# Kernel optimization log

Measured on AMD Instinct MI355X. Metric: run time of the kernel, lower is better.

The kernel has to match this reference:

```python
import jax, jax.numpy as jnp
import numpy as np

B, IN_CH, N, DIM, PH, HID, K = 4, 128, 2048, 256, 64, 1024, 16
EPS = 1e-5


def conv1(x, w, b):
    # 1x1 Conv1d: x (B,C,N), w (O,C) -> (B,O,N)
    return jnp.einsum('oc,bcn->bon', w, x) + b[None, :, None]


def conv2(x, w, b):
    # 1x1 Conv2d: x (B,C,N,K), w (O,C) -> (B,O,N,K)
    return jnp.einsum('oc,bcnk->bonk', w, x) + b[None, :, None, None]


def bn2(x, g, beta, mean, var):
    # eval-mode BatchNorm2d over channel dim of (B,C,N,K)
    scale = g * jax.lax.rsqrt(var + EPS)
    return x * scale[None, :, None, None] + (beta - mean * scale)[None, :, None, None]


def query_knn(pos, k):
    # pos: (B,3,N). Returns (B,N,K) indices of k nearest neighbors (incl. self).
    p = jnp.transpose(pos, (0, 2, 1))                     # (B,N,3)
    sq = jnp.sum(p * p, axis=-1)                          # (B,N)
    dist = sq[:, :, None] + sq[:, None, :] - 2.0 * jnp.einsum('bnc,bmc->bnm', p, p)
    _, idx = jax.lax.top_k(-dist, k)                      # smallest distances first
    return idx


def group(feat, idx):
    # feat: (B,C,N), idx: (B,N,K) -> (B,C,N,K) where out[b,c,i,k]=feat[b,c,idx[b,i,k]]
    b, c, n = feat.shape
    k = idx.shape[-1]
    ib = jnp.broadcast_to(idx.reshape(b, 1, n * k), (b, c, n * k))
    return jnp.take_along_axis(feat, ib, axis=2).reshape(b, c, n, k)


def setup_inputs() -> dict:
    key = jax.random.key(0)
    ks = jax.random.split(key, 12)
    s = 0.02
    return {
        'x': jax.random.normal(ks[0], (B, IN_CH, N), jnp.float32),
        'pos': jax.random.normal(ks[1], (B, 3, N), jnp.float32),
        'ls_w': jax.random.normal(ks[2], (DIM, IN_CH), jnp.float32) * s,
        'ls_b': jnp.zeros((DIM,), jnp.float32),
        'kw': jax.random.normal(ks[3], (DIM, DIM), jnp.float32) * s,
        'kb': jnp.zeros((DIM,), jnp.float32),
        'qw': jax.random.normal(ks[4], (DIM, DIM), jnp.float32) * s,
        'qb': jnp.zeros((DIM,), jnp.float32),
        'vw': jax.random.normal(ks[5], (DIM, DIM), jnp.float32) * s,
        'vb': jnp.zeros((DIM,), jnp.float32),
        'pw1': jax.random.normal(ks[6], (PH, 3), jnp.float32) * s,
        'pb1': jnp.zeros((PH,), jnp.float32),
        'pg': jnp.ones((PH,), jnp.float32),
        'pbeta': jnp.zeros((PH,), jnp.float32),
        'pmean': jnp.zeros((PH,), jnp.float32),
        'pvar': jnp.ones((PH,), jnp.float32),
        'pw2': jax.random.normal(ks[7], (DIM, PH), jnp.float32) * s,
        'pb2': jnp.zeros((DIM,), jnp.float32),
        'aw1': jax.random.normal(ks[8], (HID, DIM), jnp.float32) * s,
        'ab1': jnp.zeros((HID,), jnp.float32),
        'ag': jnp.ones((HID,), jnp.float32),
        'abeta': jnp.zeros((HID,), jnp.float32),
        'amean': jnp.zeros((HID,), jnp.float32),
        'avar': jnp.ones((HID,), jnp.float32),
        'aw2': jax.random.normal(ks[9], (DIM, HID), jnp.float32) * s,
        'ab2': jnp.zeros((DIM,), jnp.float32),
        'lw': jax.random.normal(ks[10], (IN_CH, DIM), jnp.float32) * s,
        'lb': jnp.zeros((IN_CH,), jnp.float32),
    }


def reference(x, pos, ls_w, ls_b, kw, kb, qw, qb, vw, vb,
              pw1, pb1, pg, pbeta, pmean, pvar, pw2, pb2,
              aw1, ab1, ag, abeta, amean, avar, aw2, ab2, lw, lb):
    identity = x
    h = conv1(x, ls_w, ls_b)                              # (B,DIM,N)
    idx = query_knn(pos, K)                               # (B,N,K) int32
    key_f = group(conv1(h, kw, kb), idx)                  # (B,DIM,N,K)
    value = conv1(h, vw, vb)                              # (B,DIM,N)
    query = conv1(h, qw, qb)                              # (B,DIM,N)
    qk_rel = query[:, :, :, None] - key_f                 # (B,DIM,N,K)
    pos_rel = pos[:, :, :, None] - group(pos, idx)        # (B,3,N,K)
    pe = conv2(jax.nn.relu(bn2(conv2(pos_rel, pw1, pb1), pg, pbeta, pmean, pvar)), pw2, pb2)
    attn = conv2(jax.nn.relu(bn2(conv2(qk_rel + pe, aw1, ab1), ag, abeta, amean, avar)), aw2, ab2)
    attn = jax.nn.softmax(attn, axis=-1)                  # softmax over K
    val_g = group(value, idx) + pe                        # (B,DIM,N,K)
    agg = jnp.sum(attn * val_g, axis=-1)                  # (B,DIM,N)
    y = conv1(agg, lw, lb)                                # (B,IN_CH,N)
    return y + identity
```

## Files before the change

kernel.cpp:

```cpp
#include <hip/hip_runtime.h>
#include <hip/hip_bf16.h>
#include <math.h>

#define B_    4
#define CIN   128
#define NPTS  2048
#define DIM   256
#define PH    64
#define HIDN  1024
#define KNN_  16
#define BN    (B_*NPTS)
#define CC    (BN*KNN_)
#define EPS_  1e-5f

typedef __bf16 bf16;
typedef __bf16 bf16x8 __attribute__((ext_vector_type(8)));
typedef __bf16 bf16x4 __attribute__((ext_vector_type(4)));
typedef float  f32x4  __attribute__((ext_vector_type(4)));

__global__ __launch_bounds__(256) void prep_kernel(
    const float* __restrict__ ls_w, const float* __restrict__ kw,
    const float* __restrict__ qw,   const float* __restrict__ vw,
    const float* __restrict__ pw2,  const float* __restrict__ aw1,
    const float* __restrict__ aw2,  const float* __restrict__ lw,
    const float* __restrict__ pb1,  const float* __restrict__ pg,
    const float* __restrict__ pbeta,const float* __restrict__ pmean,
    const float* __restrict__ pvar,
    const float* __restrict__ ab1,  const float* __restrict__ ag,
    const float* __restrict__ abeta,const float* __restrict__ amean,
    const float* __restrict__ avar,
    bf16* ls_wb, bf16* kwb, bf16* qwb, bf16* vwb,
    bf16* pw2b, bf16* aw1b, bf16* aw2b, bf16* lwb,
    float* pe_scale, float* pe_shift, float* at_scale, float* at_shift)
{
  long e = (long)blockIdx.x * 256 + threadIdx.x;
  if (e < 32768)  { ls_wb[e] = (bf16)ls_w[e]; return; } e -= 32768;
  if (e < 65536)  { kwb[e]   = (bf16)kw[e];   return; } e -= 65536;
  if (e < 65536)  { qwb[e]   = (bf16)qw[e];   return; } e -= 65536;
  if (e < 65536)  { vwb[e]   = (bf16)vw[e];   return; } e -= 65536;
  if (e < 16384)  { pw2b[e]  = (bf16)pw2[e];  return; } e -= 16384;
  if (e < 262144) { aw1b[e]  = (bf16)aw1[e];  return; } e -= 262144;
  if (e < 262144) { aw2b[e]  = (bf16)aw2[e];  return; } e -= 262144;
  if (e < 32768)  { lwb[e]   = (bf16)lw[e];   return; } e -= 32768;
  if (e < 64) {
    float sc = pg[e] * rsqrtf(pvar[e] + EPS_);
    pe_scale[e] = sc;
    pe_shift[e] = sc * pb1[e] + pbeta[e] - pmean[e] * sc;
    return;
  } e -= 64;
  if (e < 1024) {
    float sc = ag[e] * rsqrtf(avar[e] + EPS_);
    at_scale[e] = sc;
    at_shift[e] = sc * ab1[e] + abeta[e] - amean[e] * sc;
  }
}

__global__ __launch_bounds__(256) void transpose_x_kernel(
    const float* __restrict__ x, bf16* __restrict__ xT)
{
  long e = (long)blockIdx.x * 256 + threadIdx.x;
  int ch = (int)(e & (CIN - 1));
  long i = e >> 7;
  int n = (int)(i & (NPTS - 1));
  int b = (int)(i >> 11);
  xT[e] = (bf16)x[((long)b * CIN + ch) * NPTS + n];
}

__global__ __launch_bounds__(256) void knn_kernel(
    const float* __restrict__ pos, int* __restrict__ idx_out)
{
  __shared__ float px[NPTS], py[NPTS], pz[NPTS];
  const int tid = threadIdx.x;
  const int lane = tid & 63, wave = tid >> 6;
  const int q = blockIdx.x * 4 + wave;
  const int b = q >> 11;
  const int n = q & (NPTS - 1);
  const float* p = pos + (long)b * 3 * NPTS;
  for (int j = tid; j < NPTS; j += 256) {
    px[j] = p[j]; py[j] = p[NPTS + j]; pz[j] = p[2 * NPTS + j];
  }
  __syncthreads();
  float qx = px[n], qy = py[n], qz = pz[n];
  float qs = qx * qx + qy * qy + qz * qz;
  float d[32];
#pragma unroll
  for (int j = 0; j < 32; ++j) {
    int pt = j * 64 + lane;
    float x = px[pt], y = py[pt], z = pz[pt];
    float s2 = x * x + y * y + z * z;
    float dt = qx * x + qy * y + qz * z;
    d[j] = qs + s2 - 2.f * dt;
  }
  for (int r = 0; r < KNN_; ++r) {
    float bv = 1e30f; int bj = 0;
#pragma unroll
    for (int j = 0; j < 32; ++j)
      if (d[j] < bv) { bv = d[j]; bj = j; }
    int bi = bj * 64 + lane;
#pragma unroll
    for (int off = 32; off >= 1; off >>= 1) {
      float ov = __shfl_xor(bv, off);
      int   oi = __shfl_xor(bi, off);
      if (ov < bv || (ov == bv && oi < bi)) { bv = ov; bi = oi; }
    }
    if (lane == 0) idx_out[(long)q * KNN_ + r] = bi;
#pragma unroll
    for (int j = 0; j < 32; ++j)
      if (bi == j * 64 + lane) d[j] = 1e30f;
  }
}

template<int KD, bool OBF16>
__global__ __launch_bounds__(256) void gemmT_kernel(
    const bf16* __restrict__ inT, const bf16* __restrict__ Wb,
    const float* __restrict__ bias, void* __restrict__ outp, int O)
{
  const int tid = threadIdx.x;
  const int lane = tid & 63, wave = tid >> 6;
  const int row16 = lane & 15, grp = lane >> 4;
  const long i0 = (long)blockIdx.x * 64 + (wave & 1) * 32;
  const long o0 = (long)blockIdx.y * 64 + (wave >> 1) * 32;
  f32x4 acc[2][2] = {};
  const bf16* a0p = inT + (i0 + row16) * KD + grp * 8;
  const bf16* a1p = a0p + 16 * KD;
  const bf16* b0p = Wb + (o0 + row16) * KD + grp * 8;
  const bf16* b1p = b0p + 16 * KD;
#pragma unroll
  for (int ks = 0; ks < KD / 32; ++ks) {
    bf16x8 a0 = *(const bf16x8*)(a0p + ks * 32);
    bf16x8 a1 = *(const bf16x8*)(a1p + ks * 32);
    bf16x8 b0 = *(const bf16x8*)(b0p + ks * 32);
    bf16x8 b1 = *(const bf16x8*)(b1p + ks * 32);
    acc[0][0] = __builtin_amdgcn_mfma_f32_16x16x32_bf16(a0, b0, acc[0][0], 0, 0, 0);
    acc[0][1] = __builtin_amdgcn_mfma_f32_16x16x32_bf16(a0, b1, acc[0][1], 0, 0, 0);
    acc[1][0] = __builtin_amdgcn_mfma_f32_16x16x32_bf16(a1, b0, acc[1][0], 0, 0, 0);
    acc[1][1] = __builtin_amdgcn_mfma_f32_16x16x32_bf16(a1, b1, acc[1][1], 0, 0, 0);
  }
#pragma unroll
  for (int ot = 0; ot < 2; ++ot) {
    long o = o0 + ot * 16 + row16;
    float bv = bias[o];
#pragma unroll
    for (int it = 0; it < 2; ++it) {
#pragma unroll
      for (int r = 0; r < 4; ++r) {
        long i = i0 + it * 16 + grp * 4 + r;
        float v = acc[it][ot][r] + bv;
        if (OBF16) ((bf16*)outp)[i * O + o] = (bf16)v;
        else       ((float*)outp)[i * O + o] = v;
      }
    }
  }
}

__global__ __launch_bounds__(512, 4) void attn_fused_kernel(
    const bf16* __restrict__ qT, const bf16* __restrict__ kT,
    const bf16* __restrict__ vTb, const float* __restrict__ pos,
    const int* __restrict__ idx, const float* __restrict__ pw1,
    const float* __restrict__ pe_scale, const float* __restrict__ pe_shift,
    const bf16* __restrict__ pw2b, const float* __restrict__ pb2,
    const bf16* __restrict__ aw1b, const bf16* __restrict__ aw2b,
    const float* __restrict__ at_scale, const float* __restrict__ at_shift,
    const float* __restrict__ ab2, bf16* __restrict__ aggT)
{
  __shared__ __align__(16) bf16 u_lds[64][264];
  __shared__ __align__(16) bf16 tbuf[64 * 136];
  __shared__ float rel_lds[64][4];
  __shared__ int   idx_lds[64];
  bf16 (*t_lds)[136]  = (bf16(*)[136])tbuf;
  bf16 (*hid_lds)[72] = (bf16(*)[72])tbuf;

  const int tid = threadIdx.x;
  const int lane = tid & 63, wave = tid >> 6;
  const int row16 = lane & 15, grp = lane >> 4;
  const long c0 = (long)blockIdx.x * 64;
  const int bn0 = blockIdx.x * 4;
  const int b = bn0 >> 11;
  const float* pB = pos + (long)b * 3 * NPTS;
  const int os = wave * 32;

  if (tid < 64) {
    int nb = idx[c0 + tid];
    idx_lds[tid] = nb;
    int n = (bn0 + (tid >> 4)) & (NPTS - 1);
    rel_lds[tid][0] = pB[n] - pB[nb];
    rel_lds[tid][1] = pB[NPTS + n] - pB[NPTS + nb];
    rel_lds[tid][2] = pB[2 * NPTS + n] - pB[2 * NPTS + nb];
  }
#pragma unroll
  for (int it = 0; it < 4; ++it) {
    int id = it * 512 + tid;
    int col = id >> 5, ch16 = id & 31;
    int nb = idx[c0 + col];
    *(bf16x8*)&u_lds[col][ch16 * 8] =
        *(const bf16x8*)(kT + ((long)b * NPTS + nb) * DIM + ch16 * 8);
  }
  __syncthreads();

  {
    int c = tid & 63, jq = tid >> 6;
    float rx = rel_lds[c][0], ry = rel_lds[c][1], rz = rel_lds[c][2];
#pragma unroll
    for (int jj = 0; jj < 8; ++jj) {
      int j = jq * 8 + jj;
      float v = pw1[j * 3] * rx + pw1[j * 3 + 1] * ry + pw1[j * 3 + 2] * rz;
      v = pe_scale[j] * v + pe_shift[j];
      hid_lds[c][j] = (bf16)fmaxf(v, 0.f);
    }
  }
  __syncthreads();

  f32x4 accpe[4][2] = {};
#pragma unroll
  for (int ks = 0; ks < 2; ++ks) {
    bf16x8 ah[4];
#pragma unroll
    for (int ct = 0; ct < 4; ++ct)
      ah[ct] = *(const bf16x8*)&hid_lds[ct * 16 + row16][ks * 32 + grp * 8];
#pragma unroll
    for (int ot = 0; ot < 2; ++ot) {
      bf16x8 bw = *(const bf16x8*)(pw2b + (long)(os + ot * 16 + row16) * PH + ks * 32 + grp * 8);
#pragma unroll
      for (int ct = 0; ct < 4; ++ct)
        accpe[ct][ot] = __builtin_amdgcn_mfma_f32_16x16x32_bf16(ah[ct], bw, accpe[ct][ot], 0, 0, 0);
    }
  }

  bf16x4 pe_bf[4][2];
#pragma unroll
  for (int ot = 0; ot < 2; ++ot) {
    int o = os + ot * 16 + row16;
    float pb2v = pb2[o];
#pragma unroll
    for (int ct = 0; ct < 4; ++ct) {
      float qv = (float)qT[(long)(bn0 + ct) * DIM + o];
#pragma unroll
      for (int r = 0; r < 4; ++r) {
        int c = ct * 16 + grp * 4 + r;
        float pev = accpe[ct][ot][r] + pb2v;
        float kv = (float)u_lds[c][o];
        u_lds[c][o] = (bf16)(qv - kv + pev);
        pe_bf[ct][ot][r] = (bf16)pev;
      }
    }
  }
  __syncthreads();

  const int hs16 = wave * 16;
  f32x4 acc2[4][2] = {};
  for (int jc = 0; jc < 8; ++jc) {
    const int hg = jc * 128 + hs16;
    f32x4 acc1[4] = {};
#pragma unroll
    for (int ks = 0; ks < 8; ++ks) {
      bf16x8 bu[4];
#pragma unroll
      for (int ct = 0; ct < 4; ++ct)
        bu[ct] = *(const bf16x8*)&u_lds[ct * 16 + row16][ks * 32 + grp * 8];
      bf16x8 aw = *(const bf16x8*)(aw1b + (long)(hg + row16) * DIM + ks * 32 + grp * 8);
#pragma unroll
      for (int ct = 0; ct < 4; ++ct)
        acc1[ct] = __builtin_amdgcn_mfma_f32_16x16x32_bf16(aw, bu[ct], acc1[ct], 0, 0, 0);
    }
    {
      f32x4 sc4 = *(const f32x4*)&at_scale[hg + grp * 4];
      f32x4 sh4 = *(const f32x4*)&at_shift[hg + grp * 4];
#pragma unroll
      for (int ct = 0; ct < 4; ++ct) {
        bf16x4 pk;
#pragma unroll
        for (int r = 0; r < 4; ++r) {
          float v = sc4[r] * acc1[ct][r] + sh4[r];
          pk[r] = (bf16)fmaxf(v, 0.f);
        }
        *(bf16x4*)&t_lds[ct * 16 + row16][hs16 + grp * 4] = pk;
      }
    }
    __syncthreads();
#pragma unroll
    for (int ks2 = 0; ks2 < 4; ++ks2) {
      bf16x8 a2[4], b2;
#pragma unroll
      for (int ct = 0; ct < 4; ++ct)
        a2[ct] = *(const bf16x8*)&t_lds[ct * 16 + row16][ks2 * 32 + grp * 8];
#pragma unroll
      for (int ot = 0; ot < 2; ++ot) {
        b2 = *(const bf16x8*)(aw2b + (long)(os + ot * 16 + row16) * HIDN + jc * 128 + ks2 * 32 + grp * 8);
#pragma unroll
        for (int ct = 0; ct < 4; ++ct)
          acc2[ct][ot] = __builtin_amdgcn_mfma_f32_16x16x32_bf16(a2[ct], b2, acc2[ct][ot], 0, 0, 0);
      }
    }
    __syncthreads();
  }

#pragma unroll
  for (int ct = 0; ct < 4; ++ct) {
#pragma unroll
    for (int ot = 0; ot < 2; ++ot) {
      int o = os + ot * 16 + row16;
      float ab = ab2[o];
      float l[4];
      float m = -1e30f;
#pragma unroll
      for (int r = 0; r < 4; ++r) {
        l[r] = acc2[ct][ot][r] + ab;
        m = fmaxf(m, l[r]);
      }
      m = fmaxf(m, __shfl_xor(m, 16));
      m = fmaxf(m, __shfl_xor(m, 32));
      float s = 0.f;
#pragma unroll
      for (int r = 0; r < 4; ++r) { l[r] = __expf(l[r] - m); s += l[r]; }
      s += __shfl_xor(s, 16);
      s += __shfl_xor(s, 32);
      float inv = 1.f / s;
      float agg = 0.f;
#pragma unroll
      for (int r = 0; r < 4; ++r) {
        int c = ct * 16 + grp * 4 + r;
        int nb = idx_lds[c];
        float vv = (float)vTb[((long)b * NPTS + nb) * DIM + o];
        agg += l[r] * (vv + (float)pe_bf[ct][ot][r]);
      }
      agg *= inv;
      agg += __shfl_xor(agg, 16);
      agg += __shfl_xor(agg, 32);
      if (grp == 0) aggT[(long)(bn0 + ct) * DIM + o] = (bf16)agg;
    }
  }
}

__global__ __launch_bounds__(256) void final_kernel(
    const bf16* __restrict__ aggT, const bf16* __restrict__ lwb,
    const float* __restrict__ lb, const float* __restrict__ x,
    float* __restrict__ out)
{
  const int tid = threadIdx.x;
  const int lane = tid & 63, wave = tid >> 6;
  const int row16 = lane & 15, grp = lane >> 4;
  const long i0 = (long)blockIdx.x * 64 + (wave & 1) * 32;
  const int o0 = blockIdx.y * 64 + (wave >> 1) * 32;
  f32x4 acc[2][2] = {};
  const bf16* a0p = aggT + (i0 + row16) * DIM + grp * 8;
  const bf16* a1p = a0p + 16 * DIM;
  const bf16* b0p = lwb + (long)(o0 + row16) * DIM + grp * 8;
  const bf16* b1p = b0p + 16 * DIM;
#pragma unroll
  for (int ks = 0; ks < 8; ++ks) {
    bf16x8 a0 = *(const bf16x8*)(a0p + ks * 32);
    bf16x8 a1 = *(const bf16x8*)(a1p + ks * 32);
    bf16x8 b0 = *(const bf16x8*)(b0p + ks * 32);
    bf16x8 b1 = *(const bf16x8*)(b1p + ks * 32);
    acc[0][0] = __builtin_amdgcn_mfma_f32_16x16x32_bf16(a0, b0, acc[0][0], 0, 0, 0);
    acc[0][1] = __builtin_amdgcn_mfma_f32_16x16x32_bf16(a0, b1, acc[0][1], 0, 0, 0);
    acc[1][0] = __builtin_amdgcn_mfma_f32_16x16x32_bf16(a1, b0, acc[1][0], 0, 0, 0);
    acc[1][1] = __builtin_amdgcn_mfma_f32_16x16x32_bf16(a1, b1, acc[1][1], 0, 0, 0);
  }
#pragma unroll
  for (int ot = 0; ot < 2; ++ot) {
    int o = o0 + ot * 16 + row16;
    float bv = lb[o];
#pragma unroll
    for (int it = 0; it < 2; ++it) {
#pragma unroll
      for (int r = 0; r < 4; ++r) {
        long i = i0 + it * 16 + grp * 4 + r;
        int bb = (int)(i >> 11);
        int n = (int)(i & (NPTS - 1));
        long off = ((long)bb * CIN + o) * NPTS + n;
        out[off] = acc[it][ot][r] + bv + x[off];
      }
    }
  }
}

extern "C" void kernel_launch(void* const* d_in, const int* in_sizes, int n_in,
                              void* d_out, int out_size, void* d_ws, size_t ws_size,
                              hipStream_t stream)
{
  const float* x     = (const float*)d_in[0];
  const float* pos   = (const float*)d_in[1];
  const float* ls_w  = (const float*)d_in[2];
  const float* ls_b  = (const float*)d_in[3];
  const float* kw    = (const float*)d_in[4];
  const float* kb    = (const float*)d_in[5];
  const float* qw    = (const float*)d_in[6];
  const float* qb    = (const float*)d_in[7];
  const float* vw    = (const float*)d_in[8];
  const float* vb    = (const float*)d_in[9];
  const float* pw1   = (const float*)d_in[10];
  const float* pb1   = (const float*)d_in[11];
  const float* pg    = (const float*)d_in[12];
  const float* pbeta = (const float*)d_in[13];
  const float* pmean = (const float*)d_in[14];
  const float* pvar  = (const float*)d_in[15];
  const float* pw2   = (const float*)d_in[16];
  const float* pb2   = (const float*)d_in[17];
  const float* aw1   = (const float*)d_in[18];
  const float* ab1   = (const float*)d_in[19];
  const float* ag    = (const float*)d_in[20];
  const float* abeta = (const float*)d_in[21];
  const float* amean = (const float*)d_in[22];
  const float* avar  = (const float*)d_in[23];
  const float* aw2   = (const float*)d_in[24];
  const float* ab2   = (const float*)d_in[25];
  const float* lw    = (const float*)d_in[26];
  const float* lb    = (const float*)d_in[27];

  char* ws = (char*)d_ws;
  size_t off = 0;
  auto alloc = [&](size_t bytes) -> void* {
    void* p = ws + off;
    off = (off + bytes + 255) & ~(size_t)255;
    return p;
  };

  bf16* ls_wb = (bf16*)alloc(32768 * 2);
  bf16* kwb   = (bf16*)alloc(65536 * 2);
  bf16* qwb   = (bf16*)alloc(65536 * 2);
  bf16* vwb   = (bf16*)alloc(65536 * 2);
  bf16* pw2b  = (bf16*)alloc(16384 * 2);
  bf16* aw1b  = (bf16*)alloc(262144 * 2);
  bf16* aw2b  = (bf16*)alloc(262144 * 2);
  bf16* lwb   = (bf16*)alloc(32768 * 2);
  float* pe_scale = (float*)alloc(64 * 4);
  float* pe_shift = (float*)alloc(64 * 4);
  float* at_scale = (float*)alloc(1024 * 4);
  float* at_shift = (float*)alloc(1024 * 4);
  int*  idx  = (int*)alloc((size_t)CC * 4);
  bf16* xT   = (bf16*)alloc((size_t)BN * CIN * 2);
  bf16* hT   = (bf16*)alloc((size_t)BN * DIM * 2);
  bf16* qT   = (bf16*)alloc((size_t)BN * DIM * 2);
  bf16* kT   = (bf16*)alloc((size_t)BN * DIM * 2);
  bf16* vTb  = (bf16*)alloc((size_t)BN * DIM * 2);
  bf16* aggT = (bf16*)alloc((size_t)BN * DIM * 2);

  prep_kernel<<<dim3((803904 + 255) / 256), 256, 0, stream>>>(
      ls_w, kw, qw, vw, pw2, aw1, aw2, lw,
      pb1, pg, pbeta, pmean, pvar, ab1, ag, abeta, amean, avar,
      ls_wb, kwb, qwb, vwb, pw2b, aw1b, aw2b, lwb,
      pe_scale, pe_shift, at_scale, at_shift);

  transpose_x_kernel<<<dim3(BN * CIN / 256), 256, 0, stream>>>(x, xT);

  knn_kernel<<<dim3(BN / 4), 256, 0, stream>>>(pos, idx);

  gemmT_kernel<128, true><<<dim3(BN / 64, DIM / 64), 256, 0, stream>>>(xT, ls_wb, ls_b, hT, DIM);

  gemmT_kernel<256, true><<<dim3(BN / 64, DIM / 64), 256, 0, stream>>>(hT, qwb, qb, qT, DIM);
  gemmT_kernel<256, true><<<dim3(BN / 64, DIM / 64), 256, 0, stream>>>(hT, kwb, kb, kT, DIM);
  gemmT_kernel<256, true><<<dim3(BN / 64, DIM / 64), 256, 0, stream>>>(hT, vwb, vb, vTb, DIM);

  attn_fused_kernel<<<dim3(CC / 64), 512, 0, stream>>>(
      qT, kT, vTb, pos, idx, pw1, pe_scale, pe_shift, pw2b, pb2,
      aw1b, aw2b, at_scale, at_shift, ab2, aggT);

  final_kernel<<<dim3(BN / 64, CIN / 64), 256, 0, stream>>>(aggT, lwb, lb, x, (float*)d_out);
}
```

Measured before the change: 488.7 us.

## Swizzle LDS layouts with XOR and pair hidden-chunk MFMA loops

Replaces the padded LDS arrays in the fused attention kernel with unpadded buffers. Each 16-byte block's column index is XOR-swizzled by the row, so the bf16x8 reads avoid bank conflicts without padding. The first-stage hidden loop now handles two 128-wide hidden chunks per iteration, so each LDS read of the u operand is shared by twice as many MFMAs. The cost is more accumulator registers, which could hurt occupancy under the 512x4 launch bound.

```diff
diff --git a/kernel.cpp b/kernel.cpp
--- a/kernel.cpp
+++ b/kernel.cpp
@@ -163,16 +163,17 @@
     const float* __restrict__ at_scale, const float* __restrict__ at_shift,
     const float* __restrict__ ab2, bf16* __restrict__ aggT)
 {
-  __shared__ __align__(16) bf16 u_lds[64][264];
-  __shared__ __align__(16) bf16 tbuf[64 * 136];
+  __shared__ __align__(16) bf16 u_lds[64 * 256];
+  __shared__ __align__(16) bf16 tbuf[64 * 128];
   __shared__ float rel_lds[64][4];
   __shared__ int   idx_lds[64];
-  bf16 (*t_lds)[136]  = (bf16(*)[136])tbuf;
-  bf16 (*hid_lds)[72] = (bf16(*)[72])tbuf;
+  bf16* t_lds   = tbuf;
+  bf16* hid_lds = tbuf;
 
   const int tid = threadIdx.x;
   const int lane = tid & 63, wave = tid >> 6;
   const int row16 = lane & 15, grp = lane >> 4;
+  const int r7 = row16 & 7;
   const long c0 = (long)blockIdx.x * 64;
   const int bn0 = blockIdx.x * 4;
   const int b = bn0 >> 11;
@@ -192,7 +193,7 @@
     int id = it * 512 + tid;
     int col = id >> 5, ch16 = id & 31;
     int nb = idx[c0 + col];
-    *(bf16x8*)&u_lds[col][ch16 * 8] =
+    *(bf16x8*)&u_lds[col * 256 + ((ch16 ^ (col & 7)) << 3)] =
         *(const bf16x8*)(kT + ((long)b * NPTS + nb) * DIM + ch16 * 8);
   }
   __syncthreads();
@@ -205,7 +206,7 @@
       int j = jq * 8 + jj;
       float v = pw1[j * 3] * rx + pw1[j * 3 + 1] * ry + pw1[j * 3 + 2] * rz;
       v = pe_scale[j] * v + pe_shift[j];
-      hid_lds[c][j] = (bf16)fmaxf(v, 0.f);
+      hid_lds[c * 64 + (((j >> 3) ^ (c & 7)) << 3) + (j & 7)] = (bf16)fmaxf(v, 0.f);
     }
   }
   __syncthreads();
@@ -216,7 +217,7 @@
     bf16x8 ah[4];
 #pragma unroll
     for (int ct = 0; ct < 4; ++ct)
-      ah[ct] = *(const bf16x8*)&hid_lds[ct * 16 + row16][ks * 32 + grp * 8];
+      ah[ct] = *(const bf16x8*)&hid_lds[(ct * 16 + row16) * 64 + (((ks * 4 + grp) ^ r7) << 3)];
 #pragma unroll
     for (int ot = 0; ot < 2; ++ot) {
       bf16x8 bw = *(const bf16x8*)(pw2b + (long)(os + ot * 16 + row16) * PH + ks * 32 + grp * 8);
@@ -237,9 +238,10 @@
 #pragma unroll
       for (int r = 0; r < 4; ++r) {
         int c = ct * 16 + grp * 4 + r;
+        int ua = c * 256 + (((o >> 3) ^ (c & 7)) << 3) + (o & 7);
         float pev = accpe[ct][ot][r] + pb2v;
-        float kv = (float)u_lds[c][o];
-        u_lds[c][o] = (bf16)(qv - kv + pev);
+        float kv = (float)u_lds[ua];
+        u_lds[ua] = (bf16)(qv - kv + pev);
         pe_bf[ct][ot][r] = (bf16)pev;
       }
     }
@@ -247,51 +249,62 @@
   __syncthreads();
 
   const int hs16 = wave * 16;
+  const int tcol0 = (hs16 >> 3) << 3;
   f32x4 acc2[4][2] = {};
-  for (int jc = 0; jc < 8; ++jc) {
-    const int hg = jc * 128 + hs16;
-    f32x4 acc1[4] = {};
+  for (int jp = 0; jp < 4; ++jp) {
+    const int hg0 = (2 * jp) * 128 + hs16;
+    const int hg1 = hg0 + 128;
+    f32x4 acc1a[4] = {}, acc1b[4] = {};
 #pragma unroll
     for (int ks = 0; ks < 8; ++ks) {
       bf16x8 bu[4];
 #pragma unroll
       for (int ct = 0; ct < 4; ++ct)
-        bu[ct] = *(const bf16x8*)&u_lds[ct * 16 + row16][ks * 32 + grp * 8];
-      bf16x8 aw = *(const bf16x8*)(aw1b + (long)(hg + row16) * DIM + ks * 32 + grp * 8);
-#pragma unroll
-      for (int ct = 0; ct < 4; ++ct)
-        acc1[ct] = __builtin_amdgcn_mfma_f32_16x16x32_bf16(aw, bu[ct], acc1[ct], 0, 0, 0);
-    }
-    {
+        bu[ct] = *(const bf16x8*)&u_lds[(ct * 16 + row16) * 256 + (((ks * 4 + grp) ^ r7) << 3)];
+      bf16x8 awA = *(const bf16x8*)(aw1b + (long)(hg0 + row16) * DIM + ks * 32 + grp * 8);
+      bf16x8 awB = *(const bf16x8*)(aw1b + (long)(hg1 + row16) * DIM + ks * 32 + grp * 8);
+#pragma unroll
+      for (int ct = 0; ct < 4; ++ct) {
+        acc1a[ct] = __builtin_amdgcn_mfma_f32_16x16x32_bf16(awA, bu[ct], acc1a[ct], 0, 0, 0);
+        acc1b[ct] = __builtin_amdgcn_mfma_f32_16x16x32_bf16(awB, bu[ct], acc1b[ct], 0, 0, 0);
+      }
+    }
+#pragma unroll
+    for (int half = 0; half < 2; ++half) {
+      const int hg = half ? hg1 : hg0;
+      const int jcbase = (2 * jp + half) * 128;
       f32x4 sc4 = *(const f32x4*)&at_scale[hg + grp * 4];
       f32x4 sh4 = *(const f32x4*)&at_shift[hg + grp * 4];
 #pragma unroll
       for (int ct = 0; ct < 4; ++ct) {
+        const f32x4 a1 = half ? acc1b[ct] : acc1a[ct];
         bf16x4 pk;
 #pragma unroll
         for (int r = 0; r < 4; ++r) {
-          float v = sc4[r] * acc1[ct][r] + sh4[r];
+          float v = sc4[r] * a1[r] + sh4[r];
           pk[r] = (bf16)fmaxf(v, 0.f);
         }
-        *(bf16x4*)&t_lds[ct * 16 + row16][hs16 + grp * 4] = pk;
-      }
-    }
-    __syncthreads();
-#pragma unroll
-    for (int ks2 = 0; ks2 < 4; ++ks2) {
-      bf16x8 a2[4], b2;
-#pragma unroll
-      for (int ct = 0; ct < 4; ++ct)
-        a2[ct] = *(const bf16x8*)&t_lds[ct * 16 + row16][ks2 * 32 + grp * 8];
-#pragma unroll
-      for (int ot = 0; ot < 2; ++ot) {
-        b2 = *(const bf16x8*)(aw2b + (long)(os + ot * 16 + row16) * HIDN + jc * 128 + ks2 * 32 + grp * 8);
+        int trow = ct * 16 + row16;
+        int tblk = (wave * 2 + (grp >> 1)) ^ (trow & 7);
+        *(bf16x4*)&t_lds[trow * 128 + (tblk << 3) + ((grp & 1) << 2)] = pk;
+      }
+      __syncthreads();
+#pragma unroll
+      for (int ks2 = 0; ks2 < 4; ++ks2) {
+        bf16x8 a2[4], b2;
 #pragma unroll
         for (int ct = 0; ct < 4; ++ct)
-          acc2[ct][ot] = __builtin_amdgcn_mfma_f32_16x16x32_bf16(a2[ct], b2, acc2[ct][ot], 0, 0, 0);
-      }
-    }
-    __syncthreads();
+          a2[ct] = *(const bf16x8*)&t_lds[(ct * 16 + row16) * 128 + (((ks2 * 4 + grp) ^ r7) << 3)];
+#pragma unroll
+        for (int ot = 0; ot < 2; ++ot) {
+          b2 = *(const bf16x8*)(aw2b + (long)(os + ot * 16 + row16) * HIDN + jcbase + ks2 * 32 + grp * 8);
+#pragma unroll
+          for (int ct = 0; ct < 4; ++ct)
+            acc2[ct][ot] = __builtin_amdgcn_mfma_f32_16x16x32_bf16(a2[ct], b2, acc2[ct][ot], 0, 0, 0);
+        }
+      }
+      __syncthreads();
+    }
   }
 
 #pragma unroll
```

After: 500.4 us. 2.4% more time.
